# Kernel optimization log

Measured on AMD Instinct MI355X. Metric: run time of the kernel, lower is better.

Reference implementation:

```python
import jax, jax.numpy as jnp
import numpy as np

NEG_SLOPE = 0.2  # PyG GATv2Conv default leaky_relu slope


def _gatv2(x, src, dst, eattr, Wl, bl, Wr, br, We, att, bias, N):
    """GATv2Conv (concat heads, eval mode -> no dropout).
    x: [N, Fin], src/dst: [E], eattr: [E, Fe], att: [H, C]."""
    H, C = att.shape
    xl = (x @ Wl.T + bl).reshape(N, H, C)   # lin_l -> source features
    xr = (x @ Wr.T + br).reshape(N, H, C)   # lin_r -> target features
    ea = (eattr @ We.T).reshape(-1, H, C)   # lin_edge (no bias)
    m = xl[src] + xr[dst] + ea              # [E, H, C]
    m = jnp.where(m >= 0, m, NEG_SLOPE * m)
    logits = jnp.einsum('ehc,hc->eh', m, att)  # [E, H]
    # segment softmax over incoming edges of each target node
    lmax = jax.ops.segment_max(logits, dst, num_segments=N)  # self-loops -> nonempty
    ex = jnp.exp(logits - lmax[dst])
    denom = jax.ops.segment_sum(ex, dst, num_segments=N)
    alpha = ex / denom[dst]                 # [E, H]
    out = jax.ops.segment_sum(alpha[:, :, None] * xl[src], dst, num_segments=N)
    return out.reshape(N, H * C) + bias


def setup_inputs() -> dict:
    key = jax.random.key(0)
    ks = jax.random.split(key, 24)
    B, num_nodes, Fn, Fe, deg = 16, 5000, 64, 16, 32
    N = B * num_nodes
    E = N * deg
    s = 0.05
    inp = {
        'x': jax.random.normal(ks[0], (N, Fn), jnp.float32),
        'edge_index': jax.random.randint(ks[1], (2, E), 0, N, jnp.int64),
        'edge_attr': jax.random.normal(ks[2], (E, Fe), jnp.float32),
        'num_nodes': num_nodes,
        'W1l': jax.random.normal(ks[3], (9, Fn), jnp.float32) * s,
        'b1l': jnp.zeros((9,), jnp.float32),
        'W1r': jax.random.normal(ks[4], (9, Fn), jnp.float32) * s,
        'b1r': jnp.zeros((9,), jnp.float32),
        'We1': jax.random.normal(ks[5], (9, Fe), jnp.float32) * s,
        'att1': jax.random.normal(ks[6], (3, 3), jnp.float32) * s,
        'bias1': jnp.zeros((9,), jnp.float32),
        'W2l': jax.random.normal(ks[7], (20, 9), jnp.float32) * s,
        'b2l': jnp.zeros((20,), jnp.float32),
        'W2r': jax.random.normal(ks[8], (20, 9), jnp.float32) * s,
        'b2r': jnp.zeros((20,), jnp.float32),
        'We2': jax.random.normal(ks[9], (20, Fe), jnp.float32) * s,
        'att2': jax.random.normal(ks[10], (4, 5), jnp.float32) * s,
        'bias2': jnp.zeros((20,), jnp.float32),
        'fcW1': jax.random.normal(ks[11], (100, 20 * num_nodes), jnp.float32) * 0.01,
        'fcb1': jnp.zeros((100,), jnp.float32),
        'fcW2': jax.random.normal(ks[12], (10, 100), jnp.float32) * s,
        'fcb2': jnp.zeros((10,), jnp.float32),
        'fcW3': jax.random.normal(ks[13], (1, 10), jnp.float32) * s,
        'fcb3': jnp.zeros((1,), jnp.float32),
    }
    return inp


def reference(x, edge_index, edge_attr, num_nodes,
              W1l, b1l, W1r, b1r, We1, att1, bias1,
              W2l, b2l, W2r, b2r, We2, att2, bias2,
              fcW1, fcb1, fcW2, fcb2, fcW3, fcb3):
    N = x.shape[0]
    src0, dst0 = edge_index[0], edge_index[1]
    # add_self_loops=True, fill_value='mean': loop attr = mean of incoming edge attrs
    cnt = jax.ops.segment_sum(jnp.ones((src0.shape[0],), x.dtype), dst0, num_segments=N)
    loop_attr = jax.ops.segment_sum(edge_attr, dst0, num_segments=N) / jnp.maximum(cnt, 1.0)[:, None]
    nodes = jnp.arange(N)
    src = jnp.concatenate([src0, nodes])
    dst = jnp.concatenate([dst0, nodes])
    ea = jnp.concatenate([edge_attr, loop_attr], axis=0)

    h = _gatv2(x, src, dst, ea, W1l, b1l, W1r, b1r, We1, att1, bias1, N)
    h = jax.nn.relu(h)
    h = _gatv2(h, src, dst, ea, W2l, b2l, W2r, b2r, We2, att2, bias2, N)
    h = jax.nn.relu(h)

    B = N // num_nodes
    h = h.reshape(B, num_nodes * 20)
    h = jax.nn.relu(h @ fcW1.T + fcb1)
    h = jax.nn.relu(h @ fcW2.T + fcb2)
    return h @ fcW3.T + fcb3
```

## Files before the change

kernel.cpp:

```cpp
#include <hip/hip_runtime.h>
#include <math.h>

#define TPB   256
#define NPB   256
#define MAXNB 512
#define BCAP  10240
#define ITEMS 16
#define CPAD  16

static inline int gridFor(size_t n) { return (int)((n + TPB - 1) / TPB); }


__global__ void __launch_bounds__(TPB) k_lin1(
    const float* __restrict__ x,
    const float* __restrict__ Wl, const float* __restrict__ bl,
    const float* __restrict__ Wr, const float* __restrict__ br,
    float* __restrict__ xl, float* __restrict__ xr, int N)
{
  int idx = blockIdx.x * TPB + threadIdx.x;
  if (idx >= N * 18) return;
  int i = idx / 18, t = idx % 18;
  bool left = t < 9;
  int j = left ? t : t - 9;
  const float4* W4 = (const float4*)((left ? Wl : Wr) + j * 64);
  float s = (left ? bl : br)[j];
  const float4* xi4 = (const float4*)(x + (size_t)i * 64);
#pragma unroll
  for (int f = 0; f < 16; f++) {
    float4 xv = xi4[f], wv = W4[f];
    s = fmaf(xv.x, wv.x, s);
    s = fmaf(xv.y, wv.y, s);
    s = fmaf(xv.z, wv.z, s);
    s = fmaf(xv.w, wv.w, s);
  }
  (left ? xl : xr)[(size_t)i * 9 + j] = s;
}

__global__ void __launch_bounds__(TPB) k_lin2(
    const float* __restrict__ h1, const float* __restrict__ bias1,
    const float* __restrict__ Wl, const float* __restrict__ bl,
    const float* __restrict__ Wr, const float* __restrict__ br,
    float* __restrict__ xl, float* __restrict__ xr, int N)
{
  int idx = blockIdx.x * TPB + threadIdx.x;
  if (idx >= N * 40) return;
  int i = idx / 40, t = idx % 40;
  float hr[9];
#pragma unroll
  for (int k = 0; k < 9; k++) hr[k] = fmaxf(h1[(size_t)i * 9 + k] + bias1[k], 0.0f);
  bool left = t < 20;
  int j = left ? t : t - 20;
  const float* W = (left ? Wl : Wr) + j * 9;
  float s = (left ? bl : br)[j];
#pragma unroll
  for (int k = 0; k < 9; k++) s = fmaf(hr[k], W[k], s);
  (left ? xl : xr)[(size_t)i * 20 + j] = s;
}


__global__ void __launch_bounds__(TPB) k_bin(
    const int* __restrict__ ei, int* __restrict__ bucketCntP,
    int2* __restrict__ staging, int E, int NB)
{
  __shared__ int hist[MAXNB];
  __shared__ int base[MAXNB];
  int tid = threadIdx.x;
  size_t tile0 = (size_t)blockIdx.x * (TPB * ITEMS);
  for (int i = tid; i < NB; i += TPB) hist[i] = 0;
  __syncthreads();
  for (int it = 0; it < ITEMS; ++it) {
    size_t e = tile0 + (size_t)it * TPB + tid;
    if (e < (size_t)E) {
      int dst = ei[(size_t)E + e];
      atomicAdd(&hist[dst >> 8], 1);
    }
  }
  __syncthreads();
  for (int i = tid; i < NB; i += TPB) {
    int c = hist[i];
    base[i] = c ? atomicAdd(&bucketCntP[(size_t)i * CPAD], c) : 0;
    hist[i] = 0;
  }
  __syncthreads();
  for (int it = 0; it < ITEMS; ++it) {
    size_t e = tile0 + (size_t)it * TPB + tid;
    if (e < (size_t)E) {
      int src = ei[e];
      int dst = ei[(size_t)E + e];
      int b = dst >> 8;
      int r = atomicAdd(&hist[b], 1);
      staging[(size_t)b * BCAP + base[b] + r] =
          make_int2((int)e | ((dst & 255) << 22), src);
    }
  }
}


__global__ void __launch_bounds__(MAXNB) k_scanb(
    const int* __restrict__ bucketCntP, int* __restrict__ bucketBase, int NB)
{
  __shared__ int s[MAXNB];
  int tid = threadIdx.x;
  int v = (tid < NB) ? bucketCntP[(size_t)tid * CPAD] : 0;
  s[tid] = v;
  __syncthreads();
  for (int off = 1; off < MAXNB; off <<= 1) {
    int u = (tid >= off) ? s[tid - off] : 0;
    __syncthreads();
    s[tid] += u;
    __syncthreads();
  }
  if (tid < NB) bucketBase[tid] = s[tid] - v;
}


__global__ void __launch_bounds__(TPB) k_csr(
    const int2* __restrict__ staging, const int* __restrict__ bucketCntP,
    const int* __restrict__ bucketBase,
    int* __restrict__ rowptr, int* __restrict__ degO,
    int* __restrict__ src_csr, int* __restrict__ eid_csr, int N)
{
  int b = blockIdx.x, tid = threadIdx.x;
  int n0 = b << 8;
  int recCnt = bucketCntP[(size_t)b * CPAD];
  int ebase = bucketBase[b];
  const int2* rec = staging + (size_t)b * BCAP;
  __shared__ int deg_s[NPB];
  __shared__ int pfx[NPB];
  __shared__ int cur[NPB];
  deg_s[tid] = 0;
  __syncthreads();
  for (int r = tid; r < recCnt; r += TPB)
    atomicAdd(&deg_s[(rec[r].x >> 22) & 255], 1);
  __syncthreads();
  pfx[tid] = deg_s[tid];
  __syncthreads();
  for (int off = 1; off < NPB; off <<= 1) {
    int u = (tid >= off) ? pfx[tid - off] : 0;
    __syncthreads();
    pfx[tid] += u;
    __syncthreads();
  }
  int excl = pfx[tid] - deg_s[tid];
  int n = n0 + tid;
  if (n < N) { rowptr[n] = ebase + excl; degO[n] = deg_s[tid]; }
  cur[tid] = ebase + excl;
  __syncthreads();
  for (int r = tid; r < recCnt; r += TPB) {
    int2 rc = rec[r];
    int dl = (rc.x >> 22) & 255;
    int eid = rc.x & 0x3FFFFF;
    int pos = atomicAdd(&cur[dl], 1);
    src_csr[pos] = rc.y;
    eid_csr[pos] = eid;
  }
}


__global__ void __launch_bounds__(TPB) k_reorder(
    const int* __restrict__ eid_csr, const float4* __restrict__ eattr4,
    float4* __restrict__ eac, int E)
{
  int idx = blockIdx.x * TPB + threadIdx.x;
  int slot = idx >> 2;
  int part = idx & 3;
  if (slot >= E) return;
  int eid = eid_csr[slot];
  eac[(size_t)slot * 4 + part] = eattr4[(size_t)eid * 4 + part];
}


template <int H, int C, int L, bool SEQ>
__global__ void __launch_bounds__(TPB) k_attn(
    const int* __restrict__ rowptr, const int* __restrict__ deg,
    const int* __restrict__ src_csr, const int* __restrict__ eid_csr,
    const float* __restrict__ ea_src,
    const float* __restrict__ xl, const float* __restrict__ xr,
    const float* __restrict__ We, const float* __restrict__ att,
    const float* __restrict__ bias,
    float* __restrict__ out, int N)
{
  constexpr int HC = H * C;
  int idx = blockIdx.x * TPB + threadIdx.x;
  if (idx >= N * H * L) return;
  int l = idx & (L - 1);
  int g = idx / L;
  int n = g / H, h = g - n * H;

  float w[C][16];
#pragma unroll
  for (int c = 0; c < C; c++)
#pragma unroll
    for (int f = 0; f < 16; f++) w[c][f] = We[(h * C + c) * 16 + f];
  float attv[C], xrv[C];
#pragma unroll
  for (int c = 0; c < C; c++) {
    attv[c] = att[h * C + c];
    xrv[c] = xr[(size_t)n * HC + h * C + c];
  }

  int r0 = rowptr[n];
  int dg = deg[n];

  float mx = -3.0e38f, den = 0.0f;
  float acc[C], ea_sum[C];
#pragma unroll
  for (int c = 0; c < C; c++) { acc[c] = 0.0f; ea_sum[c] = 0.0f; }

  for (int p = l; p < dg; p += L) {
    int pos = r0 + p;
    size_t abase = SEQ ? (size_t)pos * 16 : (size_t)eid_csr[pos] * 16;
    float a[16];
    const float4* a4 = (const float4*)(ea_src + abase);
#pragma unroll
    for (int k = 0; k < 4; k++) {
      float4 v = a4[k];
      a[4 * k + 0] = v.x; a[4 * k + 1] = v.y; a[4 * k + 2] = v.z; a[4 * k + 3] = v.w;
    }
    int srcn = src_csr[pos];
    const float* xs = xl + (size_t)srcn * HC + h * C;
    float xv[C];
#pragma unroll
    for (int c = 0; c < C; c++) xv[c] = xs[c];
    float lg = 0.0f;
#pragma unroll
    for (int c = 0; c < C; c++) {
      float ea = 0.0f;
#pragma unroll
      for (int f = 0; f < 16; f++) ea = fmaf(a[f], w[c][f], ea);
      ea_sum[c] += ea;
      float m = xv[c] + xrv[c] + ea;
      m = (m >= 0.0f) ? m : 0.2f * m;
      lg = fmaf(m, attv[c], lg);
    }
    float nm = fmaxf(mx, lg);
    float s = expf(mx - nm);
    float wE = expf(lg - nm);
    den = den * s + wE;
#pragma unroll
    for (int c = 0; c < C; c++) acc[c] = fmaf(acc[c], s, wE * xv[c]);
    mx = nm;
  }

#pragma unroll
  for (int off = 1; off < L; off <<= 1) {
    float omx  = __shfl_xor(mx, off, 64);
    float oden = __shfl_xor(den, off, 64);
    float nm = fmaxf(mx, omx);
    float s1 = expf(mx - nm);
    float s2 = expf(omx - nm);
    den = den * s1 + oden * s2;
#pragma unroll
    for (int c = 0; c < C; c++) {
      float oa = __shfl_xor(acc[c], off, 64);
      float oe = __shfl_xor(ea_sum[c], off, 64);
      acc[c] = acc[c] * s1 + oa * s2;
      ea_sum[c] += oe;
    }
    mx = nm;
  }

  {
    float invd = 1.0f / fmaxf((float)dg, 1.0f);
    const float* xs = xl + (size_t)n * HC + h * C;
    float xv[C];
#pragma unroll
    for (int c = 0; c < C; c++) xv[c] = xs[c];
    float lg = 0.0f;
#pragma unroll
    for (int c = 0; c < C; c++) {
      float m = xv[c] + xrv[c] + ea_sum[c] * invd;
      m = (m >= 0.0f) ? m : 0.2f * m;
      lg = fmaf(m, attv[c], lg);
    }
    float nm = fmaxf(mx, lg);
    float s = expf(mx - nm);
    float wE = expf(lg - nm);
    den = den * s + wE;
#pragma unroll
    for (int c = 0; c < C; c++) acc[c] = fmaf(acc[c], s, wE * xv[c]);
  }

  float inv = 1.0f / den;
  float* od = out + (size_t)n * HC + h * C;
  for (int c = l; c < C; c += L) {
    float v = acc[c] * inv;
    if (bias) v = fmaxf(v + bias[h * C + c], 0.0f);
    od[c] = v;
  }
}


__global__ void __launch_bounds__(TPB) k_fc1(
    const float* __restrict__ h2, const float* __restrict__ W,
    float* __restrict__ h3, int NN, int Kc)
{
  int o = blockIdx.x;
  int ks = blockIdx.y;
  int k0 = ks * Kc;
  int k1 = min(NN, k0 + Kc);
  float acc[16];
#pragma unroll
  for (int b = 0; b < 16; b++) acc[b] = 0.0f;
  const float* wo = W + (size_t)o * NN;
  for (int k = k0 + threadIdx.x; k < k1; k += TPB) {
    float w = wo[k];
#pragma unroll
    for (int b = 0; b < 16; b++) acc[b] = fmaf(h2[(size_t)b * NN + k], w, acc[b]);
  }
#pragma unroll
  for (int b = 0; b < 16; b++) {
    float v = acc[b];
#pragma unroll
    for (int off = 32; off > 0; off >>= 1) v += __shfl_down(v, off, 64);
    if ((threadIdx.x & 63) == 0) atomicAdd(&h3[b * 100 + o], v);
  }
}

__global__ void __launch_bounds__(TPB) k_fc23(
    const float* __restrict__ h3, const float* __restrict__ fcb1,
    const float* __restrict__ W2, const float* __restrict__ b2,
    const float* __restrict__ W3, const float* __restrict__ b3,
    float* __restrict__ out, int B)
{
  __shared__ float s3[32 * 100];
  __shared__ float s4[32 * 10];
  int tid = threadIdx.x;
  for (int t = tid; t < B * 100; t += TPB)
    s3[t] = fmaxf(h3[t] + fcb1[t % 100], 0.0f);
  __syncthreads();
  if (tid < B * 10) {
    int b = tid / 10, o = tid % 10;
    float s = b2[o];
#pragma unroll
    for (int k = 0; k < 100; k++) s = fmaf(s3[b * 100 + k], W2[o * 100 + k], s);
    s4[tid] = fmaxf(s, 0.0f);
  }
  __syncthreads();
  if (tid < B) {
    float s = b3[0];
#pragma unroll
    for (int k = 0; k < 10; k++) s = fmaf(s4[tid * 10 + k], W3[k], s);
    out[tid] = s;
  }
}


extern "C" void kernel_launch(void* const* d_in, const int* in_sizes, int n_in,
                              void* d_out, int out_size, void* d_ws, size_t ws_size,
                              hipStream_t stream) {
  const float* x      = (const float*)d_in[0];
  const int*   ei     = (const int*)d_in[1];
  const float* eattr  = (const float*)d_in[2];
  const float* W1l = (const float*)d_in[4];  const float* b1l = (const float*)d_in[5];
  const float* W1r = (const float*)d_in[6];  const float* b1r = (const float*)d_in[7];
  const float* We1 = (const float*)d_in[8];  const float* att1 = (const float*)d_in[9];
  const float* bias1 = (const float*)d_in[10];
  const float* W2l = (const float*)d_in[11]; const float* b2l = (const float*)d_in[12];
  const float* W2r = (const float*)d_in[13]; const float* b2r = (const float*)d_in[14];
  const float* We2 = (const float*)d_in[15]; const float* att2 = (const float*)d_in[16];
  const float* bias2 = (const float*)d_in[17];
  const float* fcW1 = (const float*)d_in[18]; const float* fcb1 = (const float*)d_in[19];
  const float* fcW2 = (const float*)d_in[20]; const float* fcb2 = (const float*)d_in[21];
  const float* fcW3 = (const float*)d_in[22]; const float* fcb3 = (const float*)d_in[23];
  float* out = (float*)d_out;

  const int N = in_sizes[0] / 64;
  const int E = in_sizes[2] / 16;
  const int num_nodes = in_sizes[18] / (100 * 20);
  const int B = N / num_nodes;
  const int NB = (N + NPB - 1) / NPB;

  char* base = (char*)d_ws;
  size_t off = 0;
  auto alloc = [&](size_t bytes) {
    size_t o = off; off += (bytes + 63) & ~(size_t)63; return o;
  };
  size_t o_bcnt   = alloc((size_t)NB * CPAD * 4);
  size_t o_h3     = alloc((size_t)B * 100 * 4);
  size_t zeroBytes = off;
  size_t o_bbase  = alloc((size_t)NB * 4);
  size_t o_stage  = alloc((size_t)NB * BCAP * 8);
  size_t o_rowptr = alloc((size_t)N * 4);
  size_t o_deg    = alloc((size_t)N * 4);
  size_t o_srcc   = alloc((size_t)E * 4);
  size_t o_eidc   = alloc((size_t)E * 4);
  size_t o_xl1    = alloc((size_t)N * 9 * 4);
  size_t o_xr1    = alloc((size_t)N * 9 * 4);
  size_t o_xl2    = alloc((size_t)N * 20 * 4);
  size_t o_xr2    = alloc((size_t)N * 20 * 4);
  size_t o_h1     = alloc((size_t)N * 9 * 4);
  size_t o_h2     = alloc((size_t)N * 20 * 4);
  size_t o_eac    = alloc((size_t)E * 16 * 4);
  bool seq = (off <= ws_size);

  int*   bcnt   = (int*)(base + o_bcnt);
  float* h3     = (float*)(base + o_h3);
  int*   bbase  = (int*)(base + o_bbase);
  int2*  stage  = (int2*)(base + o_stage);
  int*   rowptr = (int*)(base + o_rowptr);
  int*   deg    = (int*)(base + o_deg);
  int*   srcc   = (int*)(base + o_srcc);
  int*   eidc   = (int*)(base + o_eidc);
  float* xl1    = (float*)(base + o_xl1);
  float* xr1    = (float*)(base + o_xr1);
  float* xl2    = (float*)(base + o_xl2);
  float* xr2    = (float*)(base + o_xr2);
  float* h1     = (float*)(base + o_h1);
  float* h2     = (float*)(base + o_h2);
  float* eac    = (float*)(base + o_eac);

  hipMemsetAsync(d_ws, 0, zeroBytes, stream);

  k_lin1<<<gridFor((size_t)N * 18), TPB, 0, stream>>>(x, W1l, b1l, W1r, b1r, xl1, xr1, N);

  int binBlocks = (int)(((size_t)E + TPB * ITEMS - 1) / (TPB * ITEMS));
  k_bin<<<binBlocks, TPB, 0, stream>>>(ei, bcnt, stage, E, NB);
  k_scanb<<<1, MAXNB, 0, stream>>>(bcnt, bbase, NB);
  k_csr<<<NB, TPB, 0, stream>>>(stage, bcnt, bbase, rowptr, deg, srcc, eidc, N);
  if (seq)
    k_reorder<<<gridFor((size_t)E * 4), TPB, 0, stream>>>(
        eidc, (const float4*)eattr, (float4*)eac, E);

  if (seq)
    k_attn<3, 3, 4, true><<<gridFor((size_t)N * 3 * 4), TPB, 0, stream>>>(
        rowptr, deg, srcc, eidc, eac, xl1, xr1, We1, att1, nullptr, h1, N);
  else
    k_attn<3, 3, 4, false><<<gridFor((size_t)N * 3 * 4), TPB, 0, stream>>>(
        rowptr, deg, srcc, eidc, eattr, xl1, xr1, We1, att1, nullptr, h1, N);

  k_lin2<<<gridFor((size_t)N * 40), TPB, 0, stream>>>(h1, bias1, W2l, b2l, W2r, b2r, xl2, xr2, N);

  if (seq)
    k_attn<4, 5, 4, true><<<gridFor((size_t)N * 4 * 4), TPB, 0, stream>>>(
        rowptr, deg, srcc, eidc, eac, xl2, xr2, We2, att2, bias2, h2, N);
  else
    k_attn<4, 5, 4, false><<<gridFor((size_t)N * 4 * 4), TPB, 0, stream>>>(
        rowptr, deg, srcc, eidc, eattr, xl2, xr2, We2, att2, bias2, h2, N);

  const int NN = num_nodes * 20;
  const int KS = 16;
  const int Kc = (NN + KS - 1) / KS;
  dim3 g1(100, KS);
  k_fc1<<<g1, TPB, 0, stream>>>(h2, fcW1, h3, NN, Kc);
  k_fc23<<<1, TPB, 0, stream>>>(h3, fcb1, fcW2, fcb2, fcW3, fcb3, out, B);
  (void)out_size; (void)n_in;
}
```

Baseline: 783.3 us.

## Split edge-attr dot product across lane quad with coalesced float4 loads

```diff
diff --git a/kernel.cpp b/kernel.cpp
--- a/kernel.cpp
+++ b/kernel.cpp
@@ -170,17 +170,150 @@
 }
 
 
-template <int H, int C, int L, bool SEQ>
-__global__ void __launch_bounds__(TPB) k_attn(
+template <int H, int C>
+__global__ void __launch_bounds__(TPB) k_attn4(
     const int* __restrict__ rowptr, const int* __restrict__ deg,
-    const int* __restrict__ src_csr, const int* __restrict__ eid_csr,
-    const float* __restrict__ ea_src,
+    const int* __restrict__ src_csr,
+    const float* __restrict__ eac,
     const float* __restrict__ xl, const float* __restrict__ xr,
     const float* __restrict__ We, const float* __restrict__ att,
     const float* __restrict__ bias,
     float* __restrict__ out, int N)
 {
   constexpr int HC = H * C;
+  int idx = blockIdx.x * TPB + threadIdx.x;
+  if (idx >= N * H * 4) return;
+  int l = idx & 3;
+  int g = idx >> 2;
+  int n = g / H, h = g - n * H;
+
+  float w[C][4];
+#pragma unroll
+  for (int c = 0; c < C; c++) {
+    const float* wr = We + (h * C + c) * 16 + 4 * l;
+#pragma unroll
+    for (int k = 0; k < 4; k++) w[c][k] = wr[k];
+  }
+  float attv[C], xrv[C];
+#pragma unroll
+  for (int c = 0; c < C; c++) {
+    attv[c] = att[h * C + c];
+    xrv[c] = xr[(size_t)n * HC + h * C + c];
+  }
+
+  int r0 = rowptr[n];
+  int dg = deg[n];
+
+  float mx = -3.0e38f, den = 0.0f;
+  float acc[C], ea_sum[C];
+#pragma unroll
+  for (int c = 0; c < C; c++) { acc[c] = 0.0f; ea_sum[c] = 0.0f; }
+
+  for (int p0 = 0; p0 < dg; p0 += 4) {
+    float4 zq = make_float4(0.f, 0.f, 0.f, 0.f);
+    float4 a0 = (p0 + 0 < dg) ? *(const float4*)(eac + ((size_t)(r0 + p0 + 0) * 16 + 4 * l)) : zq;
+    float4 a1 = (p0 + 1 < dg) ? *(const float4*)(eac + ((size_t)(r0 + p0 + 1) * 16 + 4 * l)) : zq;
+    float4 a2 = (p0 + 2 < dg) ? *(const float4*)(eac + ((size_t)(r0 + p0 + 2) * 16 + 4 * l)) : zq;
+    float4 a3 = (p0 + 3 < dg) ? *(const float4*)(eac + ((size_t)(r0 + p0 + 3) * 16 + 4 * l)) : zq;
+
+    int myp = p0 + l;
+    bool mine = myp < dg;
+    int pos = r0 + (mine ? myp : 0);
+    int srcn = src_csr[pos];
+    const float* xs = xl + (size_t)srcn * HC + h * C;
+    float xv[C];
+#pragma unroll
+    for (int c = 0; c < C; c++) xv[c] = xs[c];
+
+    float lg = 0.0f;
+#pragma unroll
+    for (int c = 0; c < C; c++) {
+      float d0 = fmaf(a0.w, w[c][3], fmaf(a0.z, w[c][2], fmaf(a0.y, w[c][1], a0.x * w[c][0])));
+      float d1 = fmaf(a1.w, w[c][3], fmaf(a1.z, w[c][2], fmaf(a1.y, w[c][1], a1.x * w[c][0])));
+      float d2 = fmaf(a2.w, w[c][3], fmaf(a2.z, w[c][2], fmaf(a2.y, w[c][1], a2.x * w[c][0])));
+      float d3 = fmaf(a3.w, w[c][3], fmaf(a3.z, w[c][2], fmaf(a3.y, w[c][1], a3.x * w[c][0])));
+      d0 += __shfl_xor(d0, 1, 4);  d1 += __shfl_xor(d1, 1, 4);
+      d2 += __shfl_xor(d2, 1, 4);  d3 += __shfl_xor(d3, 1, 4);
+      d0 += __shfl_xor(d0, 2, 4);  d1 += __shfl_xor(d1, 2, 4);
+      d2 += __shfl_xor(d2, 2, 4);  d3 += __shfl_xor(d3, 2, 4);
+      float eav = (l & 2) ? ((l & 1) ? d3 : d2) : ((l & 1) ? d1 : d0);
+      ea_sum[c] += mine ? eav : 0.0f;
+      float m = xv[c] + xrv[c] + eav;
+      m = (m >= 0.0f) ? m : 0.2f * m;
+      lg = fmaf(m, attv[c], lg);
+    }
+    if (mine) {
+      float nm = fmaxf(mx, lg);
+      float s = expf(mx - nm);
+      float wE = expf(lg - nm);
+      den = den * s + wE;
+#pragma unroll
+      for (int c = 0; c < C; c++) acc[c] = fmaf(acc[c], s, wE * xv[c]);
+      mx = nm;
+    }
+  }
+
+#pragma unroll
+  for (int off = 1; off < 4; off <<= 1) {
+    float omx  = __shfl_xor(mx, off, 4);
+    float oden = __shfl_xor(den, off, 4);
+    float nm = fmaxf(mx, omx);
+    float s1 = expf(mx - nm);
+    float s2 = expf(omx - nm);
+    den = den * s1 + oden * s2;
+#pragma unroll
+    for (int c = 0; c < C; c++) {
+      float oa = __shfl_xor(acc[c], off, 4);
+      float oe = __shfl_xor(ea_sum[c], off, 4);
+      acc[c] = acc[c] * s1 + oa * s2;
+      ea_sum[c] += oe;
+    }
+    mx = nm;
+  }
+
+  {
+    float invd = 1.0f / fmaxf((float)dg, 1.0f);
+    const float* xs = xl + (size_t)n * HC + h * C;
+    float xv[C];
+#pragma unroll
+    for (int c = 0; c < C; c++) xv[c] = xs[c];
+    float lg = 0.0f;
+#pragma unroll
+    for (int c = 0; c < C; c++) {
+      float m = xv[c] + xrv[c] + ea_sum[c] * invd;
+      m = (m >= 0.0f) ? m : 0.2f * m;
+      lg = fmaf(m, attv[c], lg);
+    }
+    float nm = fmaxf(mx, lg);
+    float s = expf(mx - nm);
+    float wE = expf(lg - nm);
+    den = den * s + wE;
+#pragma unroll
+    for (int c = 0; c < C; c++) acc[c] = fmaf(acc[c], s, wE * xv[c]);
+  }
+
+  float inv = 1.0f / den;
+  float* od = out + (size_t)n * HC + h * C;
+  for (int c = l; c < C; c += 4) {
+    float v = acc[c] * inv;
+    if (bias) v = fmaxf(v + bias[h * C + c], 0.0f);
+    od[c] = v;
+  }
+}
+
+
+template <int H, int C>
+__global__ void __launch_bounds__(TPB) k_attn_raw(
+    const int* __restrict__ rowptr, const int* __restrict__ deg,
+    const int* __restrict__ src_csr, const int* __restrict__ eid_csr,
+    const float* __restrict__ eattr,
+    const float* __restrict__ xl, const float* __restrict__ xr,
+    const float* __restrict__ We, const float* __restrict__ att,
+    const float* __restrict__ bias,
+    float* __restrict__ out, int N)
+{
+  constexpr int HC = H * C;
+  constexpr int L = 4;
   int idx = blockIdx.x * TPB + threadIdx.x;
   if (idx >= N * H * L) return;
   int l = idx & (L - 1);
@@ -201,7 +334,6 @@
 
   int r0 = rowptr[n];
   int dg = deg[n];
-
   float mx = -3.0e38f, den = 0.0f;
   float acc[C], ea_sum[C];
 #pragma unroll
@@ -209,9 +341,8 @@
 
   for (int p = l; p < dg; p += L) {
     int pos = r0 + p;
-    size_t abase = SEQ ? (size_t)pos * 16 : (size_t)eid_csr[pos] * 16;
     float a[16];
-    const float4* a4 = (const float4*)(ea_src + abase);
+    const float4* a4 = (const float4*)(eattr + (size_t)eid_csr[pos] * 16);
 #pragma unroll
     for (int k = 0; k < 4; k++) {
       float4 v = a4[k];
@@ -244,16 +375,16 @@
 
 #pragma unroll
   for (int off = 1; off < L; off <<= 1) {
-    float omx  = __shfl_xor(mx, off, 64);
-    float oden = __shfl_xor(den, off, 64);
+    float omx  = __shfl_xor(mx, off, 4);
+    float oden = __shfl_xor(den, off, 4);
     float nm = fmaxf(mx, omx);
     float s1 = expf(mx - nm);
     float s2 = expf(omx - nm);
     den = den * s1 + oden * s2;
 #pragma unroll
     for (int c = 0; c < C; c++) {
-      float oa = __shfl_xor(acc[c], off, 64);
-      float oe = __shfl_xor(ea_sum[c], off, 64);
+      float oa = __shfl_xor(acc[c], off, 4);
+      float oe = __shfl_xor(ea_sum[c], off, 4);
       acc[c] = acc[c] * s1 + oa * s2;
       ea_sum[c] += oe;
     }
@@ -423,19 +554,19 @@
         eidc, (const float4*)eattr, (float4*)eac, E);
 
   if (seq)
-    k_attn<3, 3, 4, true><<<gridFor((size_t)N * 3 * 4), TPB, 0, stream>>>(
-        rowptr, deg, srcc, eidc, eac, xl1, xr1, We1, att1, nullptr, h1, N);
+    k_attn4<3, 3><<<gridFor((size_t)N * 3 * 4), TPB, 0, stream>>>(
+        rowptr, deg, srcc, eac, xl1, xr1, We1, att1, nullptr, h1, N);
   else
-    k_attn<3, 3, 4, false><<<gridFor((size_t)N * 3 * 4), TPB, 0, stream>>>(
+    k_attn_raw<3, 3><<<gridFor((size_t)N * 3 * 4), TPB, 0, stream>>>(
         rowptr, deg, srcc, eidc, eattr, xl1, xr1, We1, att1, nullptr, h1, N);
 
   k_lin2<<<gridFor((size_t)N * 40), TPB, 0, stream>>>(h1, bias1, W2l, b2l, W2r, b2r, xl2, xr2, N);
 
   if (seq)
-    k_attn<4, 5, 4, true><<<gridFor((size_t)N * 4 * 4), TPB, 0, stream>>>(
-        rowptr, deg, srcc, eidc, eac, xl2, xr2, We2, att2, bias2, h2, N);
+    k_attn4<4, 5><<<gridFor((size_t)N * 4 * 4), TPB, 0, stream>>>(
+        rowptr, deg, srcc, eac, xl2, xr2, We2, att2, bias2, h2, N);
   else
-    k_attn<4, 5, 4, false><<<gridFor((size_t)N * 4 * 4), TPB, 0, stream>>>(
+    k_attn_raw<4, 5><<<gridFor((size_t)N * 4 * 4), TPB, 0, stream>>>(
         rowptr, deg, srcc, eidc, eattr, xl2, xr2, We2, att2, bias2, h2, N);
 
   const int NN = num_nodes * 20;
```

Result: slower. 845.6 us (+8.0%).
